# Performance work log

Measured on AMD Instinct MI355X. Metric: run time of the kernel, lower is better.

## Reference

```python
import jax, jax.numpy as jnp
import numpy as np

H = 64       # hidden size hard-coded in the module
NH = 4       # n_heads
S = 500      # stock_num
D = 10       # num_day
T = 40       # num_text (news per day)
FP = 3       # price features
FT = 512     # text embedding dim


def gru_scan(x, Wih, Whh, bih, bhh):
    """Single-sequence GRU (torch gate convention). x: (T, F) -> hidden states (T, H)."""
    gi = x @ Wih + bih  # (T, 3H) precompute input gates outside the scan

    def step(h, g):
        gh = h @ Whh + bhh
        r = jax.nn.sigmoid(g[:H] + gh[:H])
        z = jax.nn.sigmoid(g[H:2 * H] + gh[H:2 * H])
        n = jnp.tanh(g[2 * H:] + r * gh[2 * H:])
        h_new = (1.0 - z) * n + z * h
        return h_new, h_new

    h0 = jnp.zeros((H,), x.dtype)
    _, hs = jax.lax.scan(step, h0, gi)
    return hs


def attn_pool(hs, W, v):
    """Additive attention pooling over time. hs: (T, H) -> (H,)."""
    scores = jnp.tanh(hs @ W) @ v          # (T,)
    alpha = jax.nn.softmax(scores)
    return alpha @ hs


def _gru_params(key, fin, scale=0.08):
    k1, k2, k3, k4 = jax.random.split(key, 4)
    return (jax.random.normal(k1, (S, fin, 3 * H)) * scale,
            jax.random.normal(k2, (S, H, 3 * H)) * scale,
            jax.random.normal(k3, (S, 3 * H)) * scale,
            jax.random.normal(k4, (S, 3 * H)) * scale)


def _attn_params(key, scale=0.08):
    k1, k2 = jax.random.split(key)
    return (jax.random.normal(k1, (S, H, H)) * scale,
            jax.random.normal(k2, (S, H)) * scale)


def setup_inputs() -> dict:
    key = jax.random.key(0)
    ks = jax.random.split(key, 20)
    inp = {}
    inp['text_input'] = jax.random.normal(ks[0], (S, D, T, FT), dtype=jnp.float32)
    inp['price_input'] = jax.random.normal(ks[1], (S, D, FP), dtype=jnp.float32)
    inp['label'] = jax.random.randint(ks[2], (S,), 0, 2)
    inp['adj'] = jnp.ones((S, S), dtype=jnp.float32)
    inp['train'] = 0
    # per-stock stacked parameters
    (inp['Wih_p'], inp['Whh_p'], inp['bih_p'], inp['bhh_p']) = _gru_params(ks[3], FP)
    (inp['Wa_p'], inp['va_p']) = _attn_params(ks[4])
    (inp['Wih_t'], inp['Whh_t'], inp['bih_t'], inp['bhh_t']) = _gru_params(ks[5], FT)
    (inp['Wa_t'], inp['va_t']) = _attn_params(ks[6])
    (inp['Wih_s'], inp['Whh_s'], inp['bih_s'], inp['bhh_s']) = _gru_params(ks[7], H)
    (inp['Wa_s'], inp['va_s']) = _attn_params(ks[8])
    inp['Wb'] = jax.random.normal(ks[9], (S, H, H, H)) * 0.05   # Bilinear weight (out,in1,in2)
    inp['bb'] = jax.random.normal(ks[10], (S, H)) * 0.05
    inp['Wbl'] = jax.random.normal(ks[11], (S, H, 2)) * 0.08
    inp['bbl'] = jax.random.normal(ks[12], (S, 2)) * 0.08
    # shared cross-stock self-attention projections and final fc
    inp['Wq'] = jax.random.normal(ks[13], (H, H)) * 0.08
    inp['bq'] = jax.random.normal(ks[14], (H,)) * 0.08
    inp['Wk'] = jax.random.normal(ks[15], (H, H)) * 0.08
    inp['bk'] = jax.random.normal(ks[16], (H,)) * 0.08
    inp['Wf'] = jax.random.normal(ks[17], (H, 2)) * 0.08
    inp['bf'] = jax.random.normal(ks[18], (2,)) * 0.08
    return inp


def _forward(text_input, price_input, label,
             Wih_p, Whh_p, bih_p, bhh_p, Wa_p, va_p,
             Wih_t, Whh_t, bih_t, bhh_t, Wa_t, va_t,
             Wih_s, Whh_s, bih_s, bhh_s, Wa_s, va_s,
             Wb, bb, Wbl, bbl, Wq, bq, Wk, bk, Wf, bf):
    # ---- per-stock price encoder: GRU over days + attention pooling ----
    def enc_price(x, a, b, c, d, W, v):
        return attn_pool(gru_scan(x, a, b, c, d), W, v)
    x_price = jax.vmap(enc_price)(price_input, Wih_p, Whh_p, bih_p, bhh_p, Wa_p, va_p)  # (S, H)

    # ---- per-stock, per-day text encoder ----
    def enc_text_stock(xdays, a, b, c, d, W, v):
        return jax.vmap(lambda x: attn_pool(gru_scan(x, a, b, c, d), W, v))(xdays)  # (D, H)
    news = jax.vmap(enc_text_stock)(text_input, Wih_t, Whh_t, bih_t, bhh_t, Wa_t, va_t)  # (S, D, H)

    # ---- per-stock sequence encoder over days ----
    text_vec = jax.vmap(enc_price)(news, Wih_s, Whh_s, bih_s, bhh_s, Wa_s, va_s)  # (S, H)

    # ---- bilinear fusion: tanh(Bilinear(text, price)) ----
    combined = jnp.tanh(jnp.einsum('si,skij,sj->sk', text_vec, Wb, x_price) + bb)  # (S, H)

    # ---- per-stock blending head ----
    out_1 = jnp.tanh(jnp.einsum('si,sik->sk', combined, Wbl) + bbl)  # (S, 2)

    # ---- cross-stock multi-head self-attention (q,k projected, v identity) ----
    dh = H // NH
    q = (combined @ Wq + bq).reshape(S, NH, dh)
    k = (combined @ Wk + bk).reshape(S, NH, dh)
    v = combined.reshape(S, NH, dh)
    scores = jnp.einsum('shd,thd->hst', q, k) / (dh ** 0.5)
    attn = jax.nn.softmax(scores, axis=-1)
    attn_out = jnp.einsum('hst,thd->shd', attn, v).reshape(S, H)

    x = jax.nn.elu(attn_out @ Wf + bf)  # (S, 2)
    output = jax.nn.softmax(x + out_1, axis=1)
    # faithful to the original: CrossEntropyLoss applied to already-softmaxed output
    logp = jax.nn.log_softmax(output, axis=1)
    loss = -jnp.mean(logp[jnp.arange(S), label])
    return loss, output


def reference(text_input, price_input, label, adj, train,
              Wih_p, Whh_p, bih_p, bhh_p, Wa_p, va_p,
              Wih_t, Whh_t, bih_t, bhh_t, Wa_t, va_t,
              Wih_s, Whh_s, bih_s, bhh_s, Wa_s, va_s,
              Wb, bb, Wbl, bbl, Wq, bq, Wk, bk, Wf, bf):
    return _forward(text_input, price_input, label,
                    Wih_p, Whh_p, bih_p, bhh_p, Wa_p, va_p,
                    Wih_t, Whh_t, bih_t, bhh_t, Wa_t, va_t,
                    Wih_s, Whh_s, bih_s, bhh_s, Wa_s, va_s,
                    Wb, bb, Wbl, bbl, Wq, bq, Wk, bk, Wf, bf)
```

## Files before the change

kernel.cpp:

```cpp
#include <hip/hip_runtime.h>

#define Sn 500
#define Dn 10
#define Tn 40
#define FPn 3
#define FTn 512
#define Hn 64
#define G3 192
#define NHn 4

typedef __attribute__((ext_vector_type(8))) short bf8_t;
typedef __attribute__((ext_vector_type(4))) float f4_t;

__device__ __forceinline__ unsigned short f2bf(float f) {
    union { float f; unsigned int u; } v; v.f = f;
    unsigned int r = v.u + 0x7fffu + ((v.u >> 16) & 1u);
    return (unsigned short)(r >> 16);
}
__device__ __forceinline__ float bflo(unsigned int u) {
    union { unsigned int u; float f; } v; v.u = u << 16; return v.f;
}
__device__ __forceinline__ float bfhi(unsigned int u) {
    union { unsigned int u; float f; } v; v.u = u & 0xffff0000u; return v.f;
}
__device__ __forceinline__ unsigned int cvtpk(float lo, float hi) {
    unsigned int r;
    asm("v_cvt_pk_bf16_f32 %0, %1, %2" : "=v"(r) : "v"(lo), "v"(hi));
    return r;
}
__device__ __forceinline__ float sigmoidf_(float x) { return 1.f / (1.f + __expf(-x)); }
__device__ __forceinline__ float tanhf_(float x) {
    x = fminf(15.f, fmaxf(-15.f, x));
    float e = __expf(2.f * x);
    return (e - 1.f) / (e + 1.f);
}
__device__ __forceinline__ float dot8(uint4 wv, f4_t hA, f4_t hB) {
    return bflo(wv.x) * hA[0] + bfhi(wv.x) * hA[1]
         + bflo(wv.y) * hA[2] + bfhi(wv.y) * hA[3]
         + bflo(wv.z) * hB[0] + bfhi(wv.z) * hB[1]
         + bflo(wv.w) * hB[2] + bfhi(wv.w) * hB[3];
}
union bfu { bf8_t v; unsigned int u[4]; };

__global__ __launch_bounds__(256) void wih_prep(
    const float* __restrict__ Wih, unsigned short* __restrict__ wt)
{
    __shared__ float tile[64][65];
    const int bid = blockIdx.x;
    const int s = bid / 24, tlo = bid % 24;
    const int kt = tlo / 3, ct = tlo % 3;
    const int k0 = kt * 64, c0 = ct * 64;
    const int tid = threadIdx.x;

    const int c = tid & 63, r0 = tid >> 6;
    const float* src = Wih + ((size_t)s * FTn + k0) * G3 + c0 + c;
    #pragma unroll
    for (int i = 0; i < 16; ++i) {
        int r = i * 4 + r0;
        tile[c][r] = src[(size_t)r * G3];
    }
    __syncthreads();

    const int cl = tid >> 5, k2 = (tid & 31) * 2;
    unsigned int* wout = (unsigned int*)(wt + ((size_t)s * G3 + c0) * FTn + k0);
    #pragma unroll
    for (int p = 0; p < 8; ++p) {
        int col = cl + p * 8;
        wout[col * 256 + (k2 >> 1)] = cvtpk(tile[col][k2], tile[col][k2 + 1]);
    }
}

__global__ __launch_bounds__(256) void gi_gemm6(
    const float* __restrict__ text, const unsigned short* __restrict__ wt,
    const float* __restrict__ bih, float* __restrict__ gi2)
{
    __shared__ __align__(16) float Ab[2][2560];

    const int bid = blockIdx.x;
    const int xcd = bid & 7, ix = bid >> 3;
    const int swz = (xcd < 4 ? xcd * 313 : 1252 + (xcd - 4) * 312) + ix;
    const int s = swz / 5, fi = swz % 5;
    const int tid = threadIdx.x, w = tid >> 6, l = tid & 63;
    const int lr = l & 15, kg = l >> 4;

    const float* xbase = text + ((size_t)s * 400 + fi * 80) * FTn;
    const unsigned short* wtb = wt + ((size_t)s * G3 + w * 48) * FTn;

    const int c0 = tid, c1 = tid + 256, c2 = tid + 512;

    auto aload = [&](int kk, int c) -> f4_t {
        int row = c >> 3, slot = c & 7;
        return *(const f4_t*)(xbase + (size_t)row * FTn + kk * 32 + slot * 4);
    };
    auto awrite = [&](int c, f4_t v, float* buf) {
        int row = c >> 3, slot = c & 7;
        *(f4_t*)(buf + row * 32 + ((slot ^ (row & 7)) * 4)) = v;
    };
    auto afrag = [&](const float* buf, int mt) -> bf8_t {
        int row = mt * 16 + lr;
        int sw = row & 7;
        f4_t x0 = *(const f4_t*)(buf + row * 32 + ((((kg << 1)) ^ sw) << 2));
        f4_t x1 = *(const f4_t*)(buf + row * 32 + ((((kg << 1) | 1) ^ sw) << 2));
        bfu t;
        t.u[0] = cvtpk(x0[0], x0[1]); t.u[1] = cvtpk(x0[2], x0[3]);
        t.u[2] = cvtpk(x1[0], x1[1]); t.u[3] = cvtpk(x1[2], x1[3]);
        return t.v;
    };
    auto bload = [&](int kk, int nc) -> bf8_t {
        return *(const bf8_t*)(wtb + (size_t)(nc * 16 + lr) * FTn + kk * 32 + kg * 8);
    };

    f4_t acc[5][3];
    #pragma unroll
    for (int a = 0; a < 5; a++)
        #pragma unroll
        for (int b = 0; b < 3; b++) acc[a][b] = (f4_t){0.f, 0.f, 0.f, 0.f};

    f4_t a0 = aload(0, c0), a1 = aload(0, c1), a2;
    if (tid < 128) a2 = aload(0, c2);
    bf8_t bc0 = bload(0, 0), bc1 = bload(0, 1), bc2 = bload(0, 2);
    awrite(c0, a0, Ab[0]); awrite(c1, a1, Ab[0]);
    if (tid < 128) awrite(c2, a2, Ab[0]);
    __syncthreads();

    bf8_t bn0 = bc0, bn1 = bc1, bn2 = bc2;
    for (int kk = 0; kk < 16; ++kk) {
        float* cur = Ab[kk & 1];
        float* nxt = Ab[(kk & 1) ^ 1];
        if (kk < 15) {
            a0 = aload(kk + 1, c0); a1 = aload(kk + 1, c1);
            if (tid < 128) a2 = aload(kk + 1, c2);
            bn0 = bload(kk + 1, 0); bn1 = bload(kk + 1, 1); bn2 = bload(kk + 1, 2);
        }
        #pragma unroll
        for (int mt = 0; mt < 5; ++mt) {
            bf8_t af = afrag(cur, mt);
            acc[mt][0] = __builtin_amdgcn_mfma_f32_16x16x32_bf16(af, bc0, acc[mt][0], 0, 0, 0);
            acc[mt][1] = __builtin_amdgcn_mfma_f32_16x16x32_bf16(af, bc1, acc[mt][1], 0, 0, 0);
            acc[mt][2] = __builtin_amdgcn_mfma_f32_16x16x32_bf16(af, bc2, acc[mt][2], 0, 0, 0);
        }
        if (kk < 15) {
            awrite(c0, a0, nxt); awrite(c1, a1, nxt);
            if (tid < 128) awrite(c2, a2, nxt);
        }
        __syncthreads();
        bc0 = bn0; bc1 = bn1; bc2 = bn2;
    }

    const float* bihs = bih + (size_t)s * G3 + w * 48 + lr;
    #pragma unroll
    for (int nc = 0; nc < 3; ++nc) {
        const int col = w * 48 + nc * 16 + lr;
        const float bv = bihs[nc * 16];
        #pragma unroll
        for (int mt = 0; mt < 5; ++mt)
            #pragma unroll
            for (int rg = 0; rg < 4; ++rg) {
                int r = mt * 16 + kg * 4 + rg;
                int hi = (r >= 40);
                int day = fi * 2 + hi;
                int t = r - hi * 40;
                gi2[((size_t)(s * 40 + t) * 10 + day) * 192 + col] = acc[mt][nc][rg] + bv;
            }
    }
}

__global__ __launch_bounds__(64, 1) void gru_text_f(
    const float* __restrict__ gi2, const float* __restrict__ Whh,
    const float* __restrict__ bhh, const float* __restrict__ Wa,
    const float* __restrict__ va, float* __restrict__ news)
{
    __shared__ __align__(16) float hrow[16 * 68];
    __shared__ __align__(16) unsigned char waT[Hn * 128];

    const int s = blockIdx.x, l = threadIdx.x;
    const int lr = l & 15, lg = l >> 4;

    const float* Whhs = Whh + (size_t)s * Hn * G3;
    bfu bwhh[2][12];
    #pragma unroll
    for (int ks = 0; ks < 2; ++ks)
        #pragma unroll
        for (int nt = 0; nt < 12; ++nt) {
            const float* p = Whhs + (size_t)(ks * 32 + lg * 8) * G3 + nt * 16 + lr;
            float b0 = p[0], b1 = p[G3], b2 = p[2 * G3], b3 = p[3 * G3];
            float b4 = p[4 * G3], b5 = p[5 * G3], b6 = p[6 * G3], b7 = p[7 * G3];
            bwhh[ks][nt].u[0] = cvtpk(b0, b1); bwhh[ks][nt].u[1] = cvtpk(b2, b3);
            bwhh[ks][nt].u[2] = cvtpk(b4, b5); bwhh[ks][nt].u[3] = cvtpk(b6, b7);
        }
    float bhh_l[12];
    #pragma unroll
    for (int nt = 0; nt < 12; ++nt) bhh_l[nt] = bhh[(size_t)s * G3 + nt * 16 + lr];
    float va_l[4];
    #pragma unroll
    for (int nt = 0; nt < 4; ++nt) va_l[nt] = va[(size_t)s * Hn + nt * 16 + lr];

    {
        const float* Was = Wa + (size_t)s * Hn * Hn;
        for (int r = 0; r < 64; ++r) {
            int e = l + r * 64, i = e >> 6, k = e & 63;
            *(unsigned short*)(waT + k * 128 + ((2 * i) ^ ((k & 7) << 4))) = f2bf(Was[e]);
        }
        #pragma unroll
        for (int r = 0; r < 17; ++r) hrow[l + r * 64] = 0.f;
    }
    __builtin_amdgcn_wave_barrier();

    int dayoff[4];
    #pragma unroll
    for (int rr = 0; rr < 4; ++rr) {
        int d = lg * 4 + rr; if (d > 9) d = 9;
        dayoff[rr] = d * 192 + lr;
    }
    const float* gbase = gi2 + (size_t)s * 40 * 1920;

    float val[48], valn[48];
    #pragma unroll
    for (int j = 0; j < 48; ++j) val[j] = gbase[dayoff[j & 3] + (j >> 2) * 16];

    bf8_t a0f, a1f;
    {   bfu z0; z0.u[0] = 0; z0.u[1] = 0; z0.u[2] = 0; z0.u[3] = 0; a0f = z0.v; a1f = z0.v; }

    float h[4][4], accv[4][4], den[4], m[4];
    #pragma unroll
    for (int nt = 0; nt < 4; ++nt)
        #pragma unroll
        for (int rr = 0; rr < 4; ++rr) { h[nt][rr] = 0.f; accv[nt][rr] = 0.f; }
    #pragma unroll
    for (int rr = 0; rr < 4; ++rr) { den[rr] = 0.f; m[rr] = -1e30f; }

    for (int t = 0; t < Tn; ++t) {
        f4_t acc[12];
        #pragma unroll
        for (int nt = 0; nt < 12; ++nt)
            acc[nt] = (f4_t){bhh_l[nt], bhh_l[nt], bhh_l[nt], bhh_l[nt]};
        #pragma unroll
        for (int nt = 0; nt < 12; ++nt) {
            acc[nt] = __builtin_amdgcn_mfma_f32_16x16x32_bf16(a0f, bwhh[0][nt].v, acc[nt], 0, 0, 0);
            acc[nt] = __builtin_amdgcn_mfma_f32_16x16x32_bf16(a1f, bwhh[1][nt].v, acc[nt], 0, 0, 0);
        }
        {
            const int tn = (t < Tn - 1) ? t + 1 : t;
            const float* gb = gbase + (size_t)tn * 1920;
            #pragma unroll
            for (int j = 0; j < 48; ++j) valn[j] = gb[dayoff[j & 3] + (j >> 2) * 16];
        }
        #pragma unroll
        for (int nt = 0; nt < 4; ++nt)
            #pragma unroll
            for (int rr = 0; rr < 4; ++rr) {
                float r = sigmoidf_(val[nt * 4 + rr] + acc[nt][rr]);
                float z = sigmoidf_(val[(nt + 4) * 4 + rr] + acc[nt + 4][rr]);
                float n = tanhf_(val[(nt + 8) * 4 + rr] + r * acc[nt + 8][rr]);
                h[nt][rr] = (1.f - z) * n + z * h[nt][rr];
            }
        __builtin_amdgcn_wave_barrier();
        #pragma unroll
        for (int rr = 0; rr < 4; ++rr) {
            int day = lg * 4 + rr;
            if (day < Dn) {
                #pragma unroll
                for (int nt = 0; nt < 4; ++nt) hrow[day * 68 + nt * 16 + lr] = h[nt][rr];
            }
        }
        __builtin_amdgcn_wave_barrier();
        {
            const float* hp = hrow + lr * 68 + lg * 8;
            f4_t x0 = *(const f4_t*)hp,        x1 = *(const f4_t*)(hp + 4);
            f4_t y0 = *(const f4_t*)(hp + 32), y1 = *(const f4_t*)(hp + 36);
            bfu t0, t1;
            t0.u[0] = cvtpk(x0[0], x0[1]); t0.u[1] = cvtpk(x0[2], x0[3]);
            t0.u[2] = cvtpk(x1[0], x1[1]); t0.u[3] = cvtpk(x1[2], x1[3]);
            t1.u[0] = cvtpk(y0[0], y0[1]); t1.u[1] = cvtpk(y0[2], y0[3]);
            t1.u[2] = cvtpk(y1[0], y1[1]); t1.u[3] = cvtpk(y1[2], y1[3]);
            a0f = t0.v; a1f = t1.v;
        }
        f4_t sc[4];
        #pragma unroll
        for (int nt = 0; nt < 4; ++nt) sc[nt] = (f4_t){0.f, 0.f, 0.f, 0.f};
        #pragma unroll
        for (int ks = 0; ks < 2; ++ks) {
            bf8_t av = ks ? a1f : a0f;
            #pragma unroll
            for (int nt = 0; nt < 4; ++nt) {
                bf8_t bwv = *(const bf8_t*)(waT + (nt * 16 + lr) * 128
                                            + ((ks * 64 + lg * 16) ^ ((lr & 7) << 4)));
                sc[nt] = __builtin_amdgcn_mfma_f32_16x16x32_bf16(av, bwv, sc[nt], 0, 0, 0);
            }
        }
        float pr[4];
        #pragma unroll
        for (int rr = 0; rr < 4; ++rr) {
            pr[rr] = tanhf_(sc[0][rr]) * va_l[0] + tanhf_(sc[1][rr]) * va_l[1]
                   + tanhf_(sc[2][rr]) * va_l[2] + tanhf_(sc[3][rr]) * va_l[3];
            pr[rr] += __shfl_xor(pr[rr], 1);
            pr[rr] += __shfl_xor(pr[rr], 2);
            pr[rr] += __shfl_xor(pr[rr], 4);
            pr[rr] += __shfl_xor(pr[rr], 8);
        }
        #pragma unroll
        for (int rr = 0; rr < 4; ++rr) {
            float mn = fmaxf(m[rr], pr[rr]);
            float s0 = __expf(m[rr] - mn);
            float p = __expf(pr[rr] - mn);
            den[rr] = den[rr] * s0 + p;
            #pragma unroll
            for (int nt = 0; nt < 4; ++nt)
                accv[nt][rr] = accv[nt][rr] * s0 + p * h[nt][rr];
            m[rr] = mn;
        }
        #pragma unroll
        for (int j = 0; j < 48; ++j) val[j] = valn[j];
    }
    #pragma unroll
    for (int rr = 0; rr < 4; ++rr) {
        int day = lg * 4 + rr;
        if (day < Dn) {
            float inv = 1.f / den[rr];
            #pragma unroll
            for (int nt = 0; nt < 4; ++nt)
                news[((size_t)s * Dn + day) * Hn + nt * 16 + lr] = accv[nt][rr] * inv;
        }
    }
}

__global__ __launch_bounds__(64, 1) void gru_small_f(
    const float* __restrict__ news,
    const float* __restrict__ Wih_s, const float* __restrict__ Whh_s,
    const float* __restrict__ bih_s, const float* __restrict__ bhh_s,
    const float* __restrict__ Wa_s, const float* __restrict__ va_s,
    const float* __restrict__ price, const float* __restrict__ Wih_p,
    const float* __restrict__ Whh_p, const float* __restrict__ bih_p,
    const float* __restrict__ bhh_p, const float* __restrict__ Wa_p,
    const float* __restrict__ va_p,
    float* __restrict__ tvec, float* __restrict__ xprice)
{
    __shared__ __align__(16) unsigned char sm[60928];
    unsigned char* whh2 = sm;
    unsigned char* wih2 = sm + 24576;
    unsigned char* wa2 = sm + 49152;
    float* newsL = (float*)(sm + 57600);
    float* hbuf  = (float*)(sm + 60320);
    float* priceL = (float*)(sm + 60608);

    const int s = blockIdx.x, l = threadIdx.x;

    {
        const float* W2 = Whh_s + (size_t)s * Hn * G3;
        const float* X2 = Wih_s + (size_t)s * Hn * G3;
        for (int r = 0; r < 192; ++r) {
            int e = l + r * 64, i = e / G3, j = e - i * G3;
            int off = j * 128 + ((2 * i) ^ ((j & 7) << 4));
            *(unsigned short*)(whh2 + off) = f2bf(W2[e]);
            *(unsigned short*)(wih2 + off) = f2bf(X2[e]);
        }
        const float* A2 = Wa_s + (size_t)s * Hn * Hn;
        for (int r = 0; r < 64; ++r) {
            int e = l + r * 64, i = e >> 6, k = e & 63;
            *(unsigned short*)(wa2 + k * 128 + ((2 * i) ^ ((k & 7) << 4))) = f2bf(A2[e]);
        }
        #pragma unroll
        for (int d = 0; d < Dn; ++d) newsL[d * 68 + l] = news[((size_t)s * Dn + d) * Hn + l];
        hbuf[l] = 0.f;
        if (l < 4) hbuf[64 + l] = 0.f;
    }
    __builtin_amdgcn_wave_barrier();
    {
        const float bi0 = bih_s[(size_t)s * G3 + l];
        const float bi1 = bih_s[(size_t)s * G3 + 64 + l];
        const float bi2 = bih_s[(size_t)s * G3 + 128 + l];
        const float bh0 = bhh_s[(size_t)s * G3 + l];
        const float bh1 = bhh_s[(size_t)s * G3 + 64 + l];
        const float bh2 = bhh_s[(size_t)s * G3 + 128 + l];
        const float vak = va_s[(size_t)s * Hn + l];
        const int swl = (l & 7) << 4;
        float h2 = 0.f, m2 = -1e30f, den2 = 0.f, av2 = 0.f;
        for (int t = 0; t < Dn; ++t) {
            float gh0 = bh0, gh1 = bh1, gh2 = bh2;
            float gg0 = bi0, gg1 = bi1, gg2 = bi2;
            #pragma unroll
            for (int ic = 0; ic < 8; ++ic) {
                const int off = (ic * 16) ^ swl;
                f4_t hA = *(const f4_t*)&hbuf[ic * 8];
                f4_t hB = *(const f4_t*)&hbuf[ic * 8 + 4];
                f4_t nA = *(const f4_t*)&newsL[t * 68 + ic * 8];
                f4_t nB = *(const f4_t*)&newsL[t * 68 + ic * 8 + 4];
                uint4 w0 = *(const uint4*)(whh2 + l * 128 + off);
                uint4 w1 = *(const uint4*)(whh2 + (l + 64) * 128 + off);
                uint4 w2 = *(const uint4*)(whh2 + (l + 128) * 128 + off);
                uint4 x0 = *(const uint4*)(wih2 + l * 128 + off);
                uint4 x1 = *(const uint4*)(wih2 + (l + 64) * 128 + off);
                uint4 x2 = *(const uint4*)(wih2 + (l + 128) * 128 + off);
                gh0 += dot8(w0, hA, hB); gh1 += dot8(w1, hA, hB); gh2 += dot8(w2, hA, hB);
                gg0 += dot8(x0, nA, nB); gg1 += dot8(x1, nA, nB); gg2 += dot8(x2, nA, nB);
            }
            float r = sigmoidf_(gg0 + gh0);
            float z = sigmoidf_(gg1 + gh1);
            float n = tanhf_(gg2 + r * gh2);
            h2 = (1.f - z) * n + z * h2;
            __builtin_amdgcn_wave_barrier();
            hbuf[l] = h2;
            __builtin_amdgcn_wave_barrier();
            float sk = 0.f;
            #pragma unroll
            for (int ic = 0; ic < 8; ++ic) {
                const int off = (ic * 16) ^ swl;
                uint4 wv = *(const uint4*)(wa2 + l * 128 + off);
                f4_t hA = *(const f4_t*)&hbuf[ic * 8];
                f4_t hB = *(const f4_t*)&hbuf[ic * 8 + 4];
                sk += dot8(wv, hA, hB);
            }
            float term = tanhf_(sk) * vak;
            #pragma unroll
            for (int off = 32; off; off >>= 1) term += __shfl_xor(term, off);
            float mn = fmaxf(m2, term);
            float s0 = __expf(m2 - mn);
            float p = __expf(term - mn);
            den2 = den2 * s0 + p;
            av2 = av2 * s0 + p * h2;
            m2 = mn;
        }
        tvec[(size_t)s * Hn + l] = av2 / den2;
    }
    __builtin_amdgcn_wave_barrier();

    {
        const float* W3 = Whh_p + (size_t)s * Hn * G3;
        for (int r = 0; r < 192; ++r) {
            int e = l + r * 64, i = e / G3, j = e - i * G3;
            *(unsigned short*)(whh2 + j * 128 + ((2 * i) ^ ((j & 7) << 4))) = f2bf(W3[e]);
        }
        const float* A3 = Wa_p + (size_t)s * Hn * Hn;
        for (int r = 0; r < 64; ++r) {
            int e = l + r * 64, i = e >> 6, k = e & 63;
            *(unsigned short*)(wa2 + k * 128 + ((2 * i) ^ ((k & 7) << 4))) = f2bf(A3[e]);
        }
        if (l < 30) priceL[l] = price[(size_t)s * 30 + l];
        hbuf[l] = 0.f;
        if (l < 4) hbuf[64 + l] = 0.f;
    }
    __builtin_amdgcn_wave_barrier();
    {
        float wp[3][3];
        #pragma unroll
        for (int i = 0; i < 3; ++i)
            #pragma unroll
            for (int g = 0; g < 3; ++g)
                wp[i][g] = Wih_p[(size_t)s * 3 * G3 + i * G3 + g * 64 + l];
        const float bi0 = bih_p[(size_t)s * G3 + l];
        const float bi1 = bih_p[(size_t)s * G3 + 64 + l];
        const float bi2 = bih_p[(size_t)s * G3 + 128 + l];
        const float bh0 = bhh_p[(size_t)s * G3 + l];
        const float bh1 = bhh_p[(size_t)s * G3 + 64 + l];
        const float bh2 = bhh_p[(size_t)s * G3 + 128 + l];
        const float vak = va_p[(size_t)s * Hn + l];
        const int swl = (l & 7) << 4;
        float h3 = 0.f, m3 = -1e30f, den3 = 0.f, av3 = 0.f;
        for (int t = 0; t < Dn; ++t) {
            float x0 = priceL[t * 3], x1 = priceL[t * 3 + 1], x2 = priceL[t * 3 + 2];
            float gg0 = bi0 + x0 * wp[0][0] + x1 * wp[1][0] + x2 * wp[2][0];
            float gg1 = bi1 + x0 * wp[0][1] + x1 * wp[1][1] + x2 * wp[2][1];
            float gg2 = bi2 + x0 * wp[0][2] + x1 * wp[1][2] + x2 * wp[2][2];
            float gh0 = bh0, gh1 = bh1, gh2 = bh2;
            #pragma unroll
            for (int ic = 0; ic < 8; ++ic) {
                const int off = (ic * 16) ^ swl;
                f4_t hA = *(const f4_t*)&hbuf[ic * 8];
                f4_t hB = *(const f4_t*)&hbuf[ic * 8 + 4];
                uint4 w0 = *(const uint4*)(whh2 + l * 128 + off);
                uint4 w1 = *(const uint4*)(whh2 + (l + 64) * 128 + off);
                uint4 w2 = *(const uint4*)(whh2 + (l + 128) * 128 + off);
                gh0 += dot8(w0, hA, hB); gh1 += dot8(w1, hA, hB); gh2 += dot8(w2, hA, hB);
            }
            float r = sigmoidf_(gg0 + gh0);
            float z = sigmoidf_(gg1 + gh1);
            float n = tanhf_(gg2 + r * gh2);
            h3 = (1.f - z) * n + z * h3;
            __builtin_amdgcn_wave_barrier();
            hbuf[l] = h3;
            __builtin_amdgcn_wave_barrier();
            float sk = 0.f;
            #pragma unroll
            for (int ic = 0; ic < 8; ++ic) {
                const int off = (ic * 16) ^ swl;
                uint4 wv = *(const uint4*)(wa2 + l * 128 + off);
                f4_t hA = *(const f4_t*)&hbuf[ic * 8];
                f4_t hB = *(const f4_t*)&hbuf[ic * 8 + 4];
                sk += dot8(wv, hA, hB);
            }
            float term = tanhf_(sk) * vak;
            #pragma unroll
            for (int off = 32; off; off >>= 1) term += __shfl_xor(term, off);
            float mn = fmaxf(m3, term);
            float s0 = __expf(m3 - mn);
            float p = __expf(term - mn);
            den3 = den3 * s0 + p;
            av3 = av3 * s0 + p * h3;
            m3 = mn;
        }
        xprice[(size_t)s * Hn + l] = av3 / den3;
    }
}

__global__ __launch_bounds__(256) void bilinear4(
    const float* __restrict__ Wb, const float* __restrict__ bb,
    const float* __restrict__ xprice, const float* __restrict__ tvec,
    float* __restrict__ combined)
{
    __shared__ __align__(16) float uT[Hn][16];
    __shared__ float tv[Hn];

    const int bid = blockIdx.x, s = bid >> 2, kq = bid & 3;
    const int tid = threadIdx.x;
    const int w = tid >> 6, l = tid & 63;
    if (tid < Hn) tv[tid] = tvec[s * Hn + tid];
    const int j4 = (l & 15) * 4;
    f4_t xq = *(const f4_t*)&xprice[s * Hn + j4];
    __syncthreads();

    const float* Wbs = Wb + (size_t)s * Hn * Hn * Hn;
    for (int g = 0; g < 64; ++g) {
        int P = kq * 1024 + w * 256 + g * 4 + (l >> 4);
        f4_t wv = *(const f4_t*)&Wbs[(size_t)P * Hn + j4];
        float dp = wv[0] * xq[0] + wv[1] * xq[1] + wv[2] * xq[2] + wv[3] * xq[3];
        dp += __shfl_xor(dp, 8);
        dp += __shfl_xor(dp, 4);
        dp += __shfl_xor(dp, 2);
        dp += __shfl_xor(dp, 1);
        if ((l & 15) == 0) { int k = P >> 6, i = P & 63; uT[i][k - kq * 16] = dp; }
    }
    __syncthreads();
    if (tid < 16) {
        const int k = kq * 16 + tid;
        float a = bb[s * Hn + k];
        for (int i = 0; i < Hn; i++) a += tv[i] * uT[i][tid];
        combined[s * Hn + k] = tanhf_(a);
    }
}

__global__ __launch_bounds__(64) void qk_proj(
    const float* __restrict__ combined, const float* __restrict__ Wq,
    const float* __restrict__ bq, const float* __restrict__ Wk,
    const float* __restrict__ bk, const float* __restrict__ Wbl,
    const float* __restrict__ bbl,
    float* __restrict__ qg, float* __restrict__ kg, float* __restrict__ out1)
{
    __shared__ float cl[Hn];
    const int s = blockIdx.x, l = threadIdx.x;
    cl[l] = combined[s * Hn + l];
    __syncthreads();
    float aq = bq[l], ak = bk[l];
    for (int i = 0; i < Hn; i++) {
        float ci = cl[i];
        aq += ci * Wq[i * Hn + l];
        ak += ci * Wk[i * Hn + l];
    }
    qg[s * Hn + l] = aq; kg[s * Hn + l] = ak;
    if (l < 2) {
        float a = bbl[s * 2 + l];
        for (int i = 0; i < Hn; i++) a += cl[i] * Wbl[(size_t)s * Hn * 2 + i * 2 + l];
        out1[s * 2 + l] = tanhf_(a);
    }
}

__global__ __launch_bounds__(256) void mhsa(
    const float* __restrict__ qg, const float* __restrict__ kg,
    const float* __restrict__ combined, const float* __restrict__ Wf,
    const float* __restrict__ bfp, const float* __restrict__ out1,
    float* __restrict__ dout)
{
    __shared__ __align__(16) float ql[Hn];
    __shared__ float sl[NHn][Sn];
    __shared__ float hsum[NHn];
    __shared__ float ao[Hn];
    __shared__ float red2[8];
    __shared__ float red3[4][Hn];

    const int sq = blockIdx.x, tid = threadIdx.x;
    if (tid < Hn) ql[tid] = qg[sq * Hn + tid];
    __syncthreads();

    for (int id = tid; id < Sn * NHn; id += 256) {
        int t = id >> 2, h = id & 3;
        const float* kp = &kg[t * Hn + h * 16];
        float a = 0.f;
        #pragma unroll
        for (int x = 0; x < 16; x += 4) {
            f4_t kv = *(const f4_t*)&kp[x];
            f4_t qv = *(const f4_t*)&ql[h * 16 + x];
            a += kv[0] * qv[0] + kv[1] * qv[1] + kv[2] * qv[2] + kv[3] * qv[3];
        }
        sl[h][t] = a * 0.25f;
    }
    __syncthreads();
    for (int h = 0; h < NHn; ++h) {
        float m = -1e30f;
        for (int t = tid; t < Sn; t += 256) m = fmaxf(m, sl[h][t]);
        for (int o = 32; o; o >>= 1) m = fmaxf(m, __shfl_xor(m, o));
        if ((tid & 63) == 0) red2[tid >> 6] = m;
        __syncthreads();
        m = fmaxf(fmaxf(red2[0], red2[1]), fmaxf(red2[2], red2[3]));
        float ps = 0.f;
        for (int t = tid; t < Sn; t += 256) { float p = __expf(sl[h][t] - m); sl[h][t] = p; ps += p; }
        for (int o = 32; o; o >>= 1) ps += __shfl_xor(ps, o);
        if ((tid & 63) == 0) red2[4 + (tid >> 6)] = ps;
        __syncthreads();
        if (tid == 0) hsum[h] = red2[4] + red2[5] + red2[6] + red2[7];
        __syncthreads();
    }
    {
        const int q = tid >> 6, j = tid & 63, h = j >> 4;
        float a = 0.f;
        for (int t = q * 125; t < q * 125 + 125; ++t) a += sl[h][t] * combined[t * Hn + j];
        red3[q][j] = a;
    }
    __syncthreads();
    if (tid < Hn)
        ao[tid] = (red3[0][tid] + red3[1][tid] + red3[2][tid] + red3[3][tid]) / hsum[tid >> 4];
    __syncthreads();
    if (tid == 0) {
        float l0 = bfp[0], l1 = bfp[1];
        for (int j = 0; j < Hn; j++) { float v = ao[j]; l0 += v * Wf[j * 2]; l1 += v * Wf[j * 2 + 1]; }
        l0 = l0 > 0.f ? l0 : __expf(l0) - 1.f;
        l1 = l1 > 0.f ? l1 : __expf(l1) - 1.f;
        l0 += out1[sq * 2]; l1 += out1[sq * 2 + 1];
        float m = fmaxf(l0, l1);
        float e0 = __expf(l0 - m), e1 = __expf(l1 - m);
        float inv = 1.f / (e0 + e1);
        dout[1 + sq * 2] = e0 * inv;
        dout[2 + sq * 2] = e1 * inv;
    }
}

__global__ __launch_bounds__(512) void loss_k(float* __restrict__ dout,
                                              const int* __restrict__ label)
{
    __shared__ float red[512];
    const int tid = threadIdx.x;
    float a = 0.f;
    if (tid < Sn) {
        float p0 = dout[1 + 2 * tid], p1 = dout[2 + 2 * tid];
        float m = fmaxf(p0, p1);
        float lse = m + __logf(__expf(p0 - m) + __expf(p1 - m));
        float pl = label[tid] ? p1 : p0;
        a = -(pl - lse);
    }
    red[tid] = a;
    __syncthreads();
    for (int o = 256; o; o >>= 1) {
        if (tid < o) red[tid] += red[tid + o];
        __syncthreads();
    }
    if (tid == 0) dout[0] = red[0] / (float)Sn;
}

extern "C" void kernel_launch(void* const* d_in, const int* in_sizes, int n_in,
                              void* d_out, int out_size, void* d_ws, size_t ws_size,
                              hipStream_t stream)
{
    const float* text  = (const float*)d_in[0];
    const float* price = (const float*)d_in[1];
    const int*   label = (const int*)  d_in[2];
    const float* Wih_p = (const float*)d_in[5];
    const float* Whh_p = (const float*)d_in[6];
    const float* bih_p = (const float*)d_in[7];
    const float* bhh_p = (const float*)d_in[8];
    const float* Wa_p  = (const float*)d_in[9];
    const float* va_p  = (const float*)d_in[10];
    const float* Wih_t = (const float*)d_in[11];
    const float* Whh_t = (const float*)d_in[12];
    const float* bih_t = (const float*)d_in[13];
    const float* bhh_t = (const float*)d_in[14];
    const float* Wa_t  = (const float*)d_in[15];
    const float* va_t  = (const float*)d_in[16];
    const float* Wih_s = (const float*)d_in[17];
    const float* Whh_s = (const float*)d_in[18];
    const float* bih_s = (const float*)d_in[19];
    const float* bhh_s = (const float*)d_in[20];
    const float* Wa_s  = (const float*)d_in[21];
    const float* va_s  = (const float*)d_in[22];
    const float* Wb    = (const float*)d_in[23];
    const float* bb    = (const float*)d_in[24];
    const float* Wbl   = (const float*)d_in[25];
    const float* bbl   = (const float*)d_in[26];
    const float* Wq    = (const float*)d_in[27];
    const float* bq    = (const float*)d_in[28];
    const float* Wk    = (const float*)d_in[29];
    const float* bk    = (const float*)d_in[30];
    const float* Wf    = (const float*)d_in[31];
    const float* bf_   = (const float*)d_in[32];

    float* ws = (float*)d_ws;
    float* news     = ws;
    float* xprice   = ws + 320000;
    float* tvec     = ws + 352000;
    float* combined = ws + 384000;
    float* qg       = ws + 416000;
    float* kg       = ws + 448000;
    float* out1     = ws + 480000;
    float* gi2      = ws + 481000;
    unsigned short* wt = (unsigned short*)(ws + 481000 + 38400000);
    float* dout = (float*)d_out;

    wih_prep<<<Sn * 24, 256, 0, stream>>>(Wih_t, wt);
    gi_gemm6<<<Sn * 5, 256, 0, stream>>>(text, wt, bih_t, gi2);
    gru_text_f<<<Sn, 64, 0, stream>>>(gi2, Whh_t, bhh_t, Wa_t, va_t, news);
    gru_small_f<<<Sn, 64, 0, stream>>>(news,
                                       Wih_s, Whh_s, bih_s, bhh_s, Wa_s, va_s,
                                       price, Wih_p, Whh_p, bih_p, bhh_p, Wa_p, va_p,
                                       tvec, xprice);
    bilinear4<<<Sn * 4, 256, 0, stream>>>(Wb, bb, xprice, tvec, combined);
    qk_proj<<<Sn, 64, 0, stream>>>(combined, Wq, bq, Wk, bk, Wbl, bbl, qg, kg, out1);
    mhsa<<<Sn, 256, 0, stream>>>(qg, kg, combined, Wf, bf_, out1, dout);
    loss_k<<<1, 512, 0, stream>>>(dout, label);
}
```

Baseline: 644.6 us.

## Fuse prep, GEMM, bilinear and projection kernels; precompute bilinear u off the recurrence path

```diff
diff --git a/kernel.cpp b/kernel.cpp
--- a/kernel.cpp
+++ b/kernel.cpp
@@ -42,387 +42,51 @@
 }
 union bfu { bf8_t v; unsigned int u[4]; };
 
-__global__ __launch_bounds__(256) void wih_prep(
-    const float* __restrict__ Wih, unsigned short* __restrict__ wt)
-{
-    __shared__ float tile[64][65];
-    const int bid = blockIdx.x;
-    const int s = bid / 24, tlo = bid % 24;
-    const int kt = tlo / 3, ct = tlo % 3;
-    const int k0 = kt * 64, c0 = ct * 64;
-    const int tid = threadIdx.x;
-
-    const int c = tid & 63, r0 = tid >> 6;
-    const float* src = Wih + ((size_t)s * FTn + k0) * G3 + c0 + c;
-    #pragma unroll
-    for (int i = 0; i < 16; ++i) {
-        int r = i * 4 + r0;
-        tile[c][r] = src[(size_t)r * G3];
-    }
-    __syncthreads();
-
-    const int cl = tid >> 5, k2 = (tid & 31) * 2;
-    unsigned int* wout = (unsigned int*)(wt + ((size_t)s * G3 + c0) * FTn + k0);
-    #pragma unroll
-    for (int p = 0; p < 8; ++p) {
-        int col = cl + p * 8;
-        wout[col * 256 + (k2 >> 1)] = cvtpk(tile[col][k2], tile[col][k2 + 1]);
-    }
-}
-
-__global__ __launch_bounds__(256) void gi_gemm6(
-    const float* __restrict__ text, const unsigned short* __restrict__ wt,
-    const float* __restrict__ bih, float* __restrict__ gi2)
-{
-    __shared__ __align__(16) float Ab[2][2560];
-
-    const int bid = blockIdx.x;
-    const int xcd = bid & 7, ix = bid >> 3;
-    const int swz = (xcd < 4 ? xcd * 313 : 1252 + (xcd - 4) * 312) + ix;
-    const int s = swz / 5, fi = swz % 5;
-    const int tid = threadIdx.x, w = tid >> 6, l = tid & 63;
-    const int lr = l & 15, kg = l >> 4;
-
-    const float* xbase = text + ((size_t)s * 400 + fi * 80) * FTn;
-    const unsigned short* wtb = wt + ((size_t)s * G3 + w * 48) * FTn;
-
-    const int c0 = tid, c1 = tid + 256, c2 = tid + 512;
-
-    auto aload = [&](int kk, int c) -> f4_t {
-        int row = c >> 3, slot = c & 7;
-        return *(const f4_t*)(xbase + (size_t)row * FTn + kk * 32 + slot * 4);
-    };
-    auto awrite = [&](int c, f4_t v, float* buf) {
-        int row = c >> 3, slot = c & 7;
-        *(f4_t*)(buf + row * 32 + ((slot ^ (row & 7)) * 4)) = v;
-    };
-    auto afrag = [&](const float* buf, int mt) -> bf8_t {
-        int row = mt * 16 + lr;
-        int sw = row & 7;
-        f4_t x0 = *(const f4_t*)(buf + row * 32 + ((((kg << 1)) ^ sw) << 2));
-        f4_t x1 = *(const f4_t*)(buf + row * 32 + ((((kg << 1) | 1) ^ sw) << 2));
-        bfu t;
-        t.u[0] = cvtpk(x0[0], x0[1]); t.u[1] = cvtpk(x0[2], x0[3]);
-        t.u[2] = cvtpk(x1[0], x1[1]); t.u[3] = cvtpk(x1[2], x1[3]);
-        return t.v;
-    };
-    auto bload = [&](int kk, int nc) -> bf8_t {
-        return *(const bf8_t*)(wtb + (size_t)(nc * 16 + lr) * FTn + kk * 32 + kg * 8);
-    };
-
-    f4_t acc[5][3];
-    #pragma unroll
-    for (int a = 0; a < 5; a++)
-        #pragma unroll
-        for (int b = 0; b < 3; b++) acc[a][b] = (f4_t){0.f, 0.f, 0.f, 0.f};
-
-    f4_t a0 = aload(0, c0), a1 = aload(0, c1), a2;
-    if (tid < 128) a2 = aload(0, c2);
-    bf8_t bc0 = bload(0, 0), bc1 = bload(0, 1), bc2 = bload(0, 2);
-    awrite(c0, a0, Ab[0]); awrite(c1, a1, Ab[0]);
-    if (tid < 128) awrite(c2, a2, Ab[0]);
-    __syncthreads();
-
-    bf8_t bn0 = bc0, bn1 = bc1, bn2 = bc2;
-    for (int kk = 0; kk < 16; ++kk) {
-        float* cur = Ab[kk & 1];
-        float* nxt = Ab[(kk & 1) ^ 1];
-        if (kk < 15) {
-            a0 = aload(kk + 1, c0); a1 = aload(kk + 1, c1);
-            if (tid < 128) a2 = aload(kk + 1, c2);
-            bn0 = bload(kk + 1, 0); bn1 = bload(kk + 1, 1); bn2 = bload(kk + 1, 2);
-        }
-        #pragma unroll
-        for (int mt = 0; mt < 5; ++mt) {
-            bf8_t af = afrag(cur, mt);
-            acc[mt][0] = __builtin_amdgcn_mfma_f32_16x16x32_bf16(af, bc0, acc[mt][0], 0, 0, 0);
-            acc[mt][1] = __builtin_amdgcn_mfma_f32_16x16x32_bf16(af, bc1, acc[mt][1], 0, 0, 0);
-            acc[mt][2] = __builtin_amdgcn_mfma_f32_16x16x32_bf16(af, bc2, acc[mt][2], 0, 0, 0);
-        }
-        if (kk < 15) {
-            awrite(c0, a0, nxt); awrite(c1, a1, nxt);
-            if (tid < 128) awrite(c2, a2, nxt);
-        }
-        __syncthreads();
-        bc0 = bn0; bc1 = bn1; bc2 = bn2;
-    }
-
-    const float* bihs = bih + (size_t)s * G3 + w * 48 + lr;
-    #pragma unroll
-    for (int nc = 0; nc < 3; ++nc) {
-        const int col = w * 48 + nc * 16 + lr;
-        const float bv = bihs[nc * 16];
-        #pragma unroll
-        for (int mt = 0; mt < 5; ++mt)
-            #pragma unroll
-            for (int rg = 0; rg < 4; ++rg) {
-                int r = mt * 16 + kg * 4 + rg;
-                int hi = (r >= 40);
-                int day = fi * 2 + hi;
-                int t = r - hi * 40;
-                gi2[((size_t)(s * 40 + t) * 10 + day) * 192 + col] = acc[mt][nc][rg] + bv;
-            }
-    }
-}
-
-__global__ __launch_bounds__(64, 1) void gru_text_f(
-    const float* __restrict__ gi2, const float* __restrict__ Whh,
-    const float* __restrict__ bhh, const float* __restrict__ Wa,
-    const float* __restrict__ va, float* __restrict__ news)
-{
-    __shared__ __align__(16) float hrow[16 * 68];
-    __shared__ __align__(16) unsigned char waT[Hn * 128];
-
-    const int s = blockIdx.x, l = threadIdx.x;
-    const int lr = l & 15, lg = l >> 4;
-
-    const float* Whhs = Whh + (size_t)s * Hn * G3;
-    bfu bwhh[2][12];
-    #pragma unroll
-    for (int ks = 0; ks < 2; ++ks)
-        #pragma unroll
-        for (int nt = 0; nt < 12; ++nt) {
-            const float* p = Whhs + (size_t)(ks * 32 + lg * 8) * G3 + nt * 16 + lr;
-            float b0 = p[0], b1 = p[G3], b2 = p[2 * G3], b3 = p[3 * G3];
-            float b4 = p[4 * G3], b5 = p[5 * G3], b6 = p[6 * G3], b7 = p[7 * G3];
-            bwhh[ks][nt].u[0] = cvtpk(b0, b1); bwhh[ks][nt].u[1] = cvtpk(b2, b3);
-            bwhh[ks][nt].u[2] = cvtpk(b4, b5); bwhh[ks][nt].u[3] = cvtpk(b6, b7);
-        }
-    float bhh_l[12];
-    #pragma unroll
-    for (int nt = 0; nt < 12; ++nt) bhh_l[nt] = bhh[(size_t)s * G3 + nt * 16 + lr];
-    float va_l[4];
-    #pragma unroll
-    for (int nt = 0; nt < 4; ++nt) va_l[nt] = va[(size_t)s * Hn + nt * 16 + lr];
-
-    {
-        const float* Was = Wa + (size_t)s * Hn * Hn;
-        for (int r = 0; r < 64; ++r) {
-            int e = l + r * 64, i = e >> 6, k = e & 63;
-            *(unsigned short*)(waT + k * 128 + ((2 * i) ^ ((k & 7) << 4))) = f2bf(Was[e]);
-        }
-        #pragma unroll
-        for (int r = 0; r < 17; ++r) hrow[l + r * 64] = 0.f;
-    }
-    __builtin_amdgcn_wave_barrier();
-
-    int dayoff[4];
-    #pragma unroll
-    for (int rr = 0; rr < 4; ++rr) {
-        int d = lg * 4 + rr; if (d > 9) d = 9;
-        dayoff[rr] = d * 192 + lr;
-    }
-    const float* gbase = gi2 + (size_t)s * 40 * 1920;
-
-    float val[48], valn[48];
-    #pragma unroll
-    for (int j = 0; j < 48; ++j) val[j] = gbase[dayoff[j & 3] + (j >> 2) * 16];
-
-    bf8_t a0f, a1f;
-    {   bfu z0; z0.u[0] = 0; z0.u[1] = 0; z0.u[2] = 0; z0.u[3] = 0; a0f = z0.v; a1f = z0.v; }
-
-    float h[4][4], accv[4][4], den[4], m[4];
-    #pragma unroll
-    for (int nt = 0; nt < 4; ++nt)
-        #pragma unroll
-        for (int rr = 0; rr < 4; ++rr) { h[nt][rr] = 0.f; accv[nt][rr] = 0.f; }
-    #pragma unroll
-    for (int rr = 0; rr < 4; ++rr) { den[rr] = 0.f; m[rr] = -1e30f; }
-
-    for (int t = 0; t < Tn; ++t) {
-        f4_t acc[12];
-        #pragma unroll
-        for (int nt = 0; nt < 12; ++nt)
-            acc[nt] = (f4_t){bhh_l[nt], bhh_l[nt], bhh_l[nt], bhh_l[nt]};
-        #pragma unroll
-        for (int nt = 0; nt < 12; ++nt) {
-            acc[nt] = __builtin_amdgcn_mfma_f32_16x16x32_bf16(a0f, bwhh[0][nt].v, acc[nt], 0, 0, 0);
-            acc[nt] = __builtin_amdgcn_mfma_f32_16x16x32_bf16(a1f, bwhh[1][nt].v, acc[nt], 0, 0, 0);
-        }
-        {
-            const int tn = (t < Tn - 1) ? t + 1 : t;
-            const float* gb = gbase + (size_t)tn * 1920;
-            #pragma unroll
-            for (int j = 0; j < 48; ++j) valn[j] = gb[dayoff[j & 3] + (j >> 2) * 16];
-        }
-        #pragma unroll
-        for (int nt = 0; nt < 4; ++nt)
-            #pragma unroll
-            for (int rr = 0; rr < 4; ++rr) {
-                float r = sigmoidf_(val[nt * 4 + rr] + acc[nt][rr]);
-                float z = sigmoidf_(val[(nt + 4) * 4 + rr] + acc[nt + 4][rr]);
-                float n = tanhf_(val[(nt + 8) * 4 + rr] + r * acc[nt + 8][rr]);
-                h[nt][rr] = (1.f - z) * n + z * h[nt][rr];
-            }
-        __builtin_amdgcn_wave_barrier();
-        #pragma unroll
-        for (int rr = 0; rr < 4; ++rr) {
-            int day = lg * 4 + rr;
-            if (day < Dn) {
-                #pragma unroll
-                for (int nt = 0; nt < 4; ++nt) hrow[day * 68 + nt * 16 + lr] = h[nt][rr];
-            }
-        }
-        __builtin_amdgcn_wave_barrier();
-        {
-            const float* hp = hrow + lr * 68 + lg * 8;
-            f4_t x0 = *(const f4_t*)hp,        x1 = *(const f4_t*)(hp + 4);
-            f4_t y0 = *(const f4_t*)(hp + 32), y1 = *(const f4_t*)(hp + 36);
-            bfu t0, t1;
-            t0.u[0] = cvtpk(x0[0], x0[1]); t0.u[1] = cvtpk(x0[2], x0[3]);
-            t0.u[2] = cvtpk(x1[0], x1[1]); t0.u[3] = cvtpk(x1[2], x1[3]);
-            t1.u[0] = cvtpk(y0[0], y0[1]); t1.u[1] = cvtpk(y0[2], y0[3]);
-            t1.u[2] = cvtpk(y1[0], y1[1]); t1.u[3] = cvtpk(y1[2], y1[3]);
-            a0f = t0.v; a1f = t1.v;
-        }
-        f4_t sc[4];
-        #pragma unroll
-        for (int nt = 0; nt < 4; ++nt) sc[nt] = (f4_t){0.f, 0.f, 0.f, 0.f};
-        #pragma unroll
-        for (int ks = 0; ks < 2; ++ks) {
-            bf8_t av = ks ? a1f : a0f;
-            #pragma unroll
-            for (int nt = 0; nt < 4; ++nt) {
-                bf8_t bwv = *(const bf8_t*)(waT + (nt * 16 + lr) * 128
-                                            + ((ks * 64 + lg * 16) ^ ((lr & 7) << 4)));
-                sc[nt] = __builtin_amdgcn_mfma_f32_16x16x32_bf16(av, bwv, sc[nt], 0, 0, 0);
-            }
-        }
-        float pr[4];
-        #pragma unroll
-        for (int rr = 0; rr < 4; ++rr) {
-            pr[rr] = tanhf_(sc[0][rr]) * va_l[0] + tanhf_(sc[1][rr]) * va_l[1]
-                   + tanhf_(sc[2][rr]) * va_l[2] + tanhf_(sc[3][rr]) * va_l[3];
-            pr[rr] += __shfl_xor(pr[rr], 1);
-            pr[rr] += __shfl_xor(pr[rr], 2);
-            pr[rr] += __shfl_xor(pr[rr], 4);
-            pr[rr] += __shfl_xor(pr[rr], 8);
-        }
-        #pragma unroll
-        for (int rr = 0; rr < 4; ++rr) {
-            float mn = fmaxf(m[rr], pr[rr]);
-            float s0 = __expf(m[rr] - mn);
-            float p = __expf(pr[rr] - mn);
-            den[rr] = den[rr] * s0 + p;
-            #pragma unroll
-            for (int nt = 0; nt < 4; ++nt)
-                accv[nt][rr] = accv[nt][rr] * s0 + p * h[nt][rr];
-            m[rr] = mn;
-        }
-        #pragma unroll
-        for (int j = 0; j < 48; ++j) val[j] = valn[j];
-    }
-    #pragma unroll
-    for (int rr = 0; rr < 4; ++rr) {
-        int day = lg * 4 + rr;
-        if (day < Dn) {
-            float inv = 1.f / den[rr];
-            #pragma unroll
-            for (int nt = 0; nt < 4; ++nt)
-                news[((size_t)s * Dn + day) * Hn + nt * 16 + lr] = accv[nt][rr] * inv;
-        }
-    }
-}
-
-__global__ __launch_bounds__(64, 1) void gru_small_f(
-    const float* __restrict__ news,
-    const float* __restrict__ Wih_s, const float* __restrict__ Whh_s,
-    const float* __restrict__ bih_s, const float* __restrict__ bhh_s,
-    const float* __restrict__ Wa_s, const float* __restrict__ va_s,
+__global__ __launch_bounds__(256) void prep_fused(
+    const float* __restrict__ Wih, unsigned short* __restrict__ wt,
     const float* __restrict__ price, const float* __restrict__ Wih_p,
     const float* __restrict__ Whh_p, const float* __restrict__ bih_p,
     const float* __restrict__ bhh_p, const float* __restrict__ Wa_p,
-    const float* __restrict__ va_p,
-    float* __restrict__ tvec, float* __restrict__ xprice)
+    const float* __restrict__ va_p, float* __restrict__ xprice)
 {
-    __shared__ __align__(16) unsigned char sm[60928];
-    unsigned char* whh2 = sm;
-    unsigned char* wih2 = sm + 24576;
-    unsigned char* wa2 = sm + 49152;
-    float* newsL = (float*)(sm + 57600);
-    float* hbuf  = (float*)(sm + 60320);
-    float* priceL = (float*)(sm + 60608);
-
-    const int s = blockIdx.x, l = threadIdx.x;
-
-    {
-        const float* W2 = Whh_s + (size_t)s * Hn * G3;
-        const float* X2 = Wih_s + (size_t)s * Hn * G3;
-        for (int r = 0; r < 192; ++r) {
-            int e = l + r * 64, i = e / G3, j = e - i * G3;
-            int off = j * 128 + ((2 * i) ^ ((j & 7) << 4));
-            *(unsigned short*)(whh2 + off) = f2bf(W2[e]);
-            *(unsigned short*)(wih2 + off) = f2bf(X2[e]);
-        }
-        const float* A2 = Wa_s + (size_t)s * Hn * Hn;
-        for (int r = 0; r < 64; ++r) {
-            int e = l + r * 64, i = e >> 6, k = e & 63;
-            *(unsigned short*)(wa2 + k * 128 + ((2 * i) ^ ((k & 7) << 4))) = f2bf(A2[e]);
-        }
-        #pragma unroll
-        for (int d = 0; d < Dn; ++d) newsL[d * 68 + l] = news[((size_t)s * Dn + d) * Hn + l];
-        hbuf[l] = 0.f;
-        if (l < 4) hbuf[64 + l] = 0.f;
-    }
-    __builtin_amdgcn_wave_barrier();
-    {
-        const float bi0 = bih_s[(size_t)s * G3 + l];
-        const float bi1 = bih_s[(size_t)s * G3 + 64 + l];
-        const float bi2 = bih_s[(size_t)s * G3 + 128 + l];
-        const float bh0 = bhh_s[(size_t)s * G3 + l];
-        const float bh1 = bhh_s[(size_t)s * G3 + 64 + l];
-        const float bh2 = bhh_s[(size_t)s * G3 + 128 + l];
-        const float vak = va_s[(size_t)s * Hn + l];
-        const int swl = (l & 7) << 4;
-        float h2 = 0.f, m2 = -1e30f, den2 = 0.f, av2 = 0.f;
-        for (int t = 0; t < Dn; ++t) {
-            float gh0 = bh0, gh1 = bh1, gh2 = bh2;
-            float gg0 = bi0, gg1 = bi1, gg2 = bi2;
-            #pragma unroll
-            for (int ic = 0; ic < 8; ++ic) {
-                const int off = (ic * 16) ^ swl;
-                f4_t hA = *(const f4_t*)&hbuf[ic * 8];
-                f4_t hB = *(const f4_t*)&hbuf[ic * 8 + 4];
-                f4_t nA = *(const f4_t*)&newsL[t * 68 + ic * 8];
-                f4_t nB = *(const f4_t*)&newsL[t * 68 + ic * 8 + 4];
-                uint4 w0 = *(const uint4*)(whh2 + l * 128 + off);
-                uint4 w1 = *(const uint4*)(whh2 + (l + 64) * 128 + off);
-                uint4 w2 = *(const uint4*)(whh2 + (l + 128) * 128 + off);
-                uint4 x0 = *(const uint4*)(wih2 + l * 128 + off);
-                uint4 x1 = *(const uint4*)(wih2 + (l + 64) * 128 + off);
-                uint4 x2 = *(const uint4*)(wih2 + (l + 128) * 128 + off);
-                gh0 += dot8(w0, hA, hB); gh1 += dot8(w1, hA, hB); gh2 += dot8(w2, hA, hB);
-                gg0 += dot8(x0, nA, nB); gg1 += dot8(x1, nA, nB); gg2 += dot8(x2, nA, nB);
-            }
-            float r = sigmoidf_(gg0 + gh0);
-            float z = sigmoidf_(gg1 + gh1);
-            float n = tanhf_(gg2 + r * gh2);
-            h2 = (1.f - z) * n + z * h2;
-            __builtin_amdgcn_wave_barrier();
-            hbuf[l] = h2;
-            __builtin_amdgcn_wave_barrier();
-            float sk = 0.f;
-            #pragma unroll
-            for (int ic = 0; ic < 8; ++ic) {
-                const int off = (ic * 16) ^ swl;
-                uint4 wv = *(const uint4*)(wa2 + l * 128 + off);
-                f4_t hA = *(const f4_t*)&hbuf[ic * 8];
-                f4_t hB = *(const f4_t*)&hbuf[ic * 8 + 4];
-                sk += dot8(wv, hA, hB);
-            }
-            float term = tanhf_(sk) * vak;
-            #pragma unroll
-            for (int off = 32; off; off >>= 1) term += __shfl_xor(term, off);
-            float mn = fmaxf(m2, term);
-            float s0 = __expf(m2 - mn);
-            float p = __expf(term - mn);
-            den2 = den2 * s0 + p;
-            av2 = av2 * s0 + p * h2;
-            m2 = mn;
-        }
-        tvec[(size_t)s * Hn + l] = av2 / den2;
-    }
-    __builtin_amdgcn_wave_barrier();
+    __shared__ float tile[64][65];
+    __shared__ __align__(16) unsigned char smp[33160];
+
+    const int bid = blockIdx.x, tid = threadIdx.x;
+
+    if (bid < 12000) {
+        const int s = bid / 24, tlo = bid % 24;
+        const int kt = tlo / 3, ct = tlo % 3;
+        const int k0 = kt * 64, c0 = ct * 64;
+
+        const int c = tid & 63, r0 = tid >> 6;
+        const float* src = Wih + ((size_t)s * FTn + k0) * G3 + c0 + c;
+        #pragma unroll
+        for (int i = 0; i < 16; ++i) {
+            int r = i * 4 + r0;
+            tile[c][r] = src[(size_t)r * G3];
+        }
+        __syncthreads();
+
+        const int cl = tid >> 5, k2 = (tid & 31) * 2;
+        unsigned int* wo = (unsigned int*)wt;
+        const int kc = (k0 >> 3) + (k2 >> 3), e2 = (k2 & 7) >> 1;
+        #pragma unroll
+        for (int p = 0; p < 8; ++p) {
+            int col = cl + p * 8;
+            wo[(size_t)s * 49152 + ((size_t)kc * G3 + c0 + col) * 4 + e2] =
+                cvtpk(tile[col][k2], tile[col][k2 + 1]);
+        }
+        return;
+    }
+
+    const int s = bid - 12000;
+    if (tid >= 64) return;
+    const int l = tid;
+    unsigned char* whh2 = smp;
+    unsigned char* wa2 = smp + 24576;
+    float* hbuf = (float*)(smp + 32768);
+    float* priceL = (float*)(smp + 33040);
 
     {
         const float* W3 = Whh_p + (size_t)s * Hn * G3;
@@ -502,64 +166,441 @@
     }
 }
 
-__global__ __launch_bounds__(256) void bilinear4(
-    const float* __restrict__ Wb, const float* __restrict__ bb,
-    const float* __restrict__ xprice, const float* __restrict__ tvec,
-    float* __restrict__ combined)
+__global__ __launch_bounds__(256) void main_fused(
+    const float* __restrict__ text, const unsigned short* __restrict__ wt,
+    const float* __restrict__ bih, float* __restrict__ gi2,
+    const float* __restrict__ Wb, const float* __restrict__ xprice,
+    float* __restrict__ u)
 {
-    __shared__ __align__(16) float uT[Hn][16];
-    __shared__ float tv[Hn];
-
-    const int bid = blockIdx.x, s = bid >> 2, kq = bid & 3;
-    const int tid = threadIdx.x;
-    const int w = tid >> 6, l = tid & 63;
-    if (tid < Hn) tv[tid] = tvec[s * Hn + tid];
-    const int j4 = (l & 15) * 4;
-    f4_t xq = *(const f4_t*)&xprice[s * Hn + j4];
-    __syncthreads();
-
-    const float* Wbs = Wb + (size_t)s * Hn * Hn * Hn;
-    for (int g = 0; g < 64; ++g) {
-        int P = kq * 1024 + w * 256 + g * 4 + (l >> 4);
-        f4_t wv = *(const f4_t*)&Wbs[(size_t)P * Hn + j4];
-        float dp = wv[0] * xq[0] + wv[1] * xq[1] + wv[2] * xq[2] + wv[3] * xq[3];
-        dp += __shfl_xor(dp, 8);
-        dp += __shfl_xor(dp, 4);
-        dp += __shfl_xor(dp, 2);
-        dp += __shfl_xor(dp, 1);
-        if ((l & 15) == 0) { int k = P >> 6, i = P & 63; uT[i][k - kq * 16] = dp; }
-    }
-    __syncthreads();
-    if (tid < 16) {
-        const int k = kq * 16 + tid;
-        float a = bb[s * Hn + k];
-        for (int i = 0; i < Hn; i++) a += tv[i] * uT[i][tid];
-        combined[s * Hn + k] = tanhf_(a);
-    }
-}
-
-__global__ __launch_bounds__(64) void qk_proj(
-    const float* __restrict__ combined, const float* __restrict__ Wq,
-    const float* __restrict__ bq, const float* __restrict__ Wk,
-    const float* __restrict__ bk, const float* __restrict__ Wbl,
-    const float* __restrict__ bbl,
-    float* __restrict__ qg, float* __restrict__ kg, float* __restrict__ out1)
+    __shared__ __align__(16) unsigned char sm[20480];
+
+    const int id = blockIdx.x;
+    const int grp = id / 9, sub = id - grp * 9;
+    const int tid = threadIdx.x, w = tid >> 6, l = tid & 63;
+
+    if (sub < 5) {
+        const int s = grp, fi = sub;
+        const int lr = l & 15, kg = l >> 4;
+        unsigned short* Ab0 = (unsigned short*)sm;
+        unsigned short* Ab1 = Ab0 + 5120;
+
+        const float* xbase = text + ((size_t)s * 400 + fi * 80) * FTn;
+        const unsigned short* wtb = wt + (size_t)s * 98304 + (size_t)(w * 48 + lr) * 8;
+
+        const int c0 = tid, c1 = tid + 256, c2 = tid + 512;
+
+        f4_t acc[5][3];
+        #pragma unroll
+        for (int a = 0; a < 5; a++)
+            #pragma unroll
+            for (int b = 0; b < 3; b++) acc[a][b] = (f4_t){0.f, 0.f, 0.f, 0.f};
+
+        f4_t pa[3], pb[3];
+        auto aload = [&](int kk) {
+            #pragma unroll
+            for (int q = 0; q < 3; ++q) {
+                int c = tid + q * 256;
+                if (q < 2 || tid < 128) {
+                    int row = c >> 3, slot = c & 7;
+                    const float* p = xbase + (size_t)row * FTn + kk * 64 + slot * 8;
+                    pa[q] = *(const f4_t*)p; pb[q] = *(const f4_t*)(p + 4);
+                }
+            }
+        };
+        auto awrite = [&](unsigned short* buf) {
+            #pragma unroll
+            for (int q = 0; q < 3; ++q) {
+                int c = tid + q * 256;
+                if (q < 2 || tid < 128) {
+                    int row = c >> 3, slot = c & 7;
+                    uint4 uu = { cvtpk(pa[q][0], pa[q][1]), cvtpk(pa[q][2], pa[q][3]),
+                                 cvtpk(pb[q][0], pb[q][1]), cvtpk(pb[q][2], pb[q][3]) };
+                    *(uint4*)(buf + row * 64 + ((slot ^ (row & 7)) * 8)) = uu;
+                }
+            }
+        };
+        auto bload = [&](int kk, int ks, int nc) -> bf8_t {
+            return *(const bf8_t*)(wtb + (size_t)((kk * 8 + ks * 4 + kg) * G3 + nc * 16) * 8);
+        };
+        auto afrag = [&](const unsigned short* buf, int mt, int ks) -> bf8_t {
+            int row = mt * 16 + lr;
+            int slot = (ks * 4 + kg) ^ (row & 7);
+            return *(const bf8_t*)(buf + row * 64 + slot * 8);
+        };
+
+        bf8_t bc[2][3], bn[2][3];
+        aload(0);
+        #pragma unroll
+        for (int ks = 0; ks < 2; ++ks)
+            #pragma unroll
+            for (int nc = 0; nc < 3; ++nc) bc[ks][nc] = bload(0, ks, nc);
+        awrite(Ab0);
+        __syncthreads();
+
+        for (int kk = 0; kk < 8; ++kk) {
+            unsigned short* cur = (kk & 1) ? Ab1 : Ab0;
+            unsigned short* nxt = (kk & 1) ? Ab0 : Ab1;
+            if (kk < 7) {
+                aload(kk + 1);
+                #pragma unroll
+                for (int ks = 0; ks < 2; ++ks)
+                    #pragma unroll
+                    for (int nc = 0; nc < 3; ++nc) bn[ks][nc] = bload(kk + 1, ks, nc);
+            }
+            #pragma unroll
+            for (int ks = 0; ks < 2; ++ks)
+                #pragma unroll
+                for (int mt = 0; mt < 5; ++mt) {
+                    bf8_t af = afrag(cur, mt, ks);
+                    acc[mt][0] = __builtin_amdgcn_mfma_f32_16x16x32_bf16(af, bc[ks][0], acc[mt][0], 0, 0, 0);
+                    acc[mt][1] = __builtin_amdgcn_mfma_f32_16x16x32_bf16(af, bc[ks][1], acc[mt][1], 0, 0, 0);
+                    acc[mt][2] = __builtin_amdgcn_mfma_f32_16x16x32_bf16(af, bc[ks][2], acc[mt][2], 0, 0, 0);
+                }
+            if (kk < 7) awrite(nxt);
+            __syncthreads();
+            #pragma unroll
+            for (int ks = 0; ks < 2; ++ks)
+                #pragma unroll
+                for (int nc = 0; nc < 3; ++nc) bc[ks][nc] = bn[ks][nc];
+        }
+
+        const float* bihs = bih + (size_t)s * G3 + w * 48 + lr;
+        #pragma unroll
+        for (int nc = 0; nc < 3; ++nc) {
+            const int col = w * 48 + nc * 16 + lr;
+            const float bv = bihs[nc * 16];
+            #pragma unroll
+            for (int mt = 0; mt < 5; ++mt)
+                #pragma unroll
+                for (int rg = 0; rg < 4; ++rg) {
+                    int r = mt * 16 + kg * 4 + rg;
+                    int hi = (r >= 40);
+                    int day = fi * 2 + hi;
+                    int t = r - hi * 40;
+                    gi2[((size_t)(s * 40 + t) * 10 + day) * 192 + col] = acc[mt][nc][rg] + bv;
+                }
+        }
+    } else {
+        const int s = grp, kq = sub - 5;
+        float* uT = (float*)sm;
+        const int j4 = (l & 15) * 4;
+        f4_t xq = *(const f4_t*)&xprice[s * Hn + j4];
+
+        const float* Wbs = Wb + (size_t)s * Hn * Hn * Hn;
+        for (int g = 0; g < 64; ++g) {
+            int P = kq * 1024 + w * 256 + g * 4 + (l >> 4);
+            f4_t wv = *(const f4_t*)&Wbs[(size_t)P * Hn + j4];
+            float dp = wv[0] * xq[0] + wv[1] * xq[1] + wv[2] * xq[2] + wv[3] * xq[3];
+            dp += __shfl_xor(dp, 8);
+            dp += __shfl_xor(dp, 4);
+            dp += __shfl_xor(dp, 2);
+            dp += __shfl_xor(dp, 1);
+            if ((l & 15) == 0) { int k = P >> 6, i = P & 63; uT[i * 17 + (k - kq * 16)] = dp; }
+        }
+        __syncthreads();
+        #pragma unroll
+        for (int r = 0; r < 4; ++r) {
+            int flat = tid + r * 256;
+            int kr = flat >> 6, i = flat & 63;
+            u[((size_t)s * 64 + kq * 16 + kr) * 64 + i] = uT[i * 17 + kr];
+        }
+    }
+}
+
+__global__ __launch_bounds__(64, 1) void gru_text_f(
+    const float* __restrict__ gi2, const float* __restrict__ Whh,
+    const float* __restrict__ bhh, const float* __restrict__ Wa,
+    const float* __restrict__ va, float* __restrict__ news)
 {
-    __shared__ float cl[Hn];
+    __shared__ __align__(16) float hrow[16 * 68];
+    __shared__ __align__(16) unsigned char waT[Hn * 128];
+
     const int s = blockIdx.x, l = threadIdx.x;
-    cl[l] = combined[s * Hn + l];
-    __syncthreads();
-    float aq = bq[l], ak = bk[l];
-    for (int i = 0; i < Hn; i++) {
-        float ci = cl[i];
-        aq += ci * Wq[i * Hn + l];
-        ak += ci * Wk[i * Hn + l];
-    }
-    qg[s * Hn + l] = aq; kg[s * Hn + l] = ak;
-    if (l < 2) {
-        float a = bbl[s * 2 + l];
-        for (int i = 0; i < Hn; i++) a += cl[i] * Wbl[(size_t)s * Hn * 2 + i * 2 + l];
-        out1[s * 2 + l] = tanhf_(a);
+    const int lr = l & 15, lg = l >> 4;
+
+    const float* Whhs = Whh + (size_t)s * Hn * G3;
+    bfu bwhh[2][12];
+    #pragma unroll
+    for (int ks = 0; ks < 2; ++ks)
+        #pragma unroll
+        for (int nt = 0; nt < 12; ++nt) {
+            const float* p = Whhs + (size_t)(ks * 32 + lg * 8) * G3 + nt * 16 + lr;
+            float b0 = p[0], b1 = p[G3], b2 = p[2 * G3], b3 = p[3 * G3];
+            float b4 = p[4 * G3], b5 = p[5 * G3], b6 = p[6 * G3], b7 = p[7 * G3];
+            bwhh[ks][nt].u[0] = cvtpk(b0, b1); bwhh[ks][nt].u[1] = cvtpk(b2, b3);
+            bwhh[ks][nt].u[2] = cvtpk(b4, b5); bwhh[ks][nt].u[3] = cvtpk(b6, b7);
+        }
+    float bhh_l[12];
+    #pragma unroll
+    for (int nt = 0; nt < 12; ++nt) bhh_l[nt] = bhh[(size_t)s * G3 + nt * 16 + lr];
+    float va_l[4];
+    #pragma unroll
+    for (int nt = 0; nt < 4; ++nt) va_l[nt] = va[(size_t)s * Hn + nt * 16 + lr];
+
+    {
+        const float* Was = Wa + (size_t)s * Hn * Hn;
+        for (int r = 0; r < 64; ++r) {
+            int e = l + r * 64, i = e >> 6, k = e & 63;
+            *(unsigned short*)(waT + k * 128 + ((2 * i) ^ ((k & 7) << 4))) = f2bf(Was[e]);
+        }
+        #pragma unroll
+        for (int r = 0; r < 17; ++r) hrow[l + r * 64] = 0.f;
+    }
+    __builtin_amdgcn_wave_barrier();
+
+    int dayoff[4];
+    #pragma unroll
+    for (int rr = 0; rr < 4; ++rr) {
+        int d = lg * 4 + rr; if (d > 9) d = 9;
+        dayoff[rr] = d * 192 + lr;
+    }
+    const float* gbase = gi2 + (size_t)s * 40 * 1920;
+
+    float val[48], valn[48];
+    #pragma unroll
+    for (int j = 0; j < 48; ++j) val[j] = gbase[dayoff[j & 3] + (j >> 2) * 16];
+
+    bf8_t a0f, a1f;
+    {   bfu z0; z0.u[0] = 0; z0.u[1] = 0; z0.u[2] = 0; z0.u[3] = 0; a0f = z0.v; a1f = z0.v; }
+
+    float h[4][4], accv[4][4], den[4], m[4];
+    #pragma unroll
+    for (int nt = 0; nt < 4; ++nt)
+        #pragma unroll
+        for (int rr = 0; rr < 4; ++rr) { h[nt][rr] = 0.f; accv[nt][rr] = 0.f; }
+    #pragma unroll
+    for (int rr = 0; rr < 4; ++rr) { den[rr] = 0.f; m[rr] = -1e30f; }
+
+    for (int t = 0; t < Tn; ++t) {
+        f4_t acc[12];
+        #pragma unroll
+        for (int nt = 0; nt < 12; ++nt)
+            acc[nt] = (f4_t){bhh_l[nt], bhh_l[nt], bhh_l[nt], bhh_l[nt]};
+        __builtin_amdgcn_s_setprio(1);
+        #pragma unroll
+        for (int nt = 0; nt < 12; ++nt) {
+            acc[nt] = __builtin_amdgcn_mfma_f32_16x16x32_bf16(a0f, bwhh[0][nt].v, acc[nt], 0, 0, 0);
+            acc[nt] = __builtin_amdgcn_mfma_f32_16x16x32_bf16(a1f, bwhh[1][nt].v, acc[nt], 0, 0, 0);
+        }
+        __builtin_amdgcn_s_setprio(0);
+        {
+            const int tn = (t < Tn - 1) ? t + 1 : t;
+            const float* gb = gbase + (size_t)tn * 1920;
+            #pragma unroll
+            for (int j = 0; j < 48; ++j) valn[j] = gb[dayoff[j & 3] + (j >> 2) * 16];
+        }
+        #pragma unroll
+        for (int nt = 0; nt < 4; ++nt)
+            #pragma unroll
+            for (int rr = 0; rr < 4; ++rr) {
+                float r = sigmoidf_(val[nt * 4 + rr] + acc[nt][rr]);
+                float z = sigmoidf_(val[(nt + 4) * 4 + rr] + acc[nt + 4][rr]);
+                float n = tanhf_(val[(nt + 8) * 4 + rr] + r * acc[nt + 8][rr]);
+                h[nt][rr] = (1.f - z) * n + z * h[nt][rr];
+            }
+        __builtin_amdgcn_wave_barrier();
+        #pragma unroll
+        for (int rr = 0; rr < 4; ++rr) {
+            int day = lg * 4 + rr;
+            if (day < Dn) {
+                #pragma unroll
+                for (int nt = 0; nt < 4; ++nt) hrow[day * 68 + nt * 16 + lr] = h[nt][rr];
+            }
+        }
+        __builtin_amdgcn_wave_barrier();
+        {
+            const float* hp = hrow + lr * 68 + lg * 8;
+            f4_t x0 = *(const f4_t*)hp,        x1 = *(const f4_t*)(hp + 4);
+            f4_t y0 = *(const f4_t*)(hp + 32), y1 = *(const f4_t*)(hp + 36);
+            bfu t0, t1;
+            t0.u[0] = cvtpk(x0[0], x0[1]); t0.u[1] = cvtpk(x0[2], x0[3]);
+            t0.u[2] = cvtpk(x1[0], x1[1]); t0.u[3] = cvtpk(x1[2], x1[3]);
+            t1.u[0] = cvtpk(y0[0], y0[1]); t1.u[1] = cvtpk(y0[2], y0[3]);
+            t1.u[2] = cvtpk(y1[0], y1[1]); t1.u[3] = cvtpk(y1[2], y1[3]);
+            a0f = t0.v; a1f = t1.v;
+        }
+        f4_t sc[4];
+        #pragma unroll
+        for (int nt = 0; nt < 4; ++nt) sc[nt] = (f4_t){0.f, 0.f, 0.f, 0.f};
+        __builtin_amdgcn_s_setprio(1);
+        #pragma unroll
+        for (int ks = 0; ks < 2; ++ks) {
+            bf8_t av = ks ? a1f : a0f;
+            #pragma unroll
+            for (int nt = 0; nt < 4; ++nt) {
+                bf8_t bwv = *(const bf8_t*)(waT + (nt * 16 + lr) * 128
+                                            + ((ks * 64 + lg * 16) ^ ((lr & 7) << 4)));
+                sc[nt] = __builtin_amdgcn_mfma_f32_16x16x32_bf16(av, bwv, sc[nt], 0, 0, 0);
+            }
+        }
+        __builtin_amdgcn_s_setprio(0);
+        float pr[4];
+        #pragma unroll
+        for (int rr = 0; rr < 4; ++rr) {
+            pr[rr] = tanhf_(sc[0][rr]) * va_l[0] + tanhf_(sc[1][rr]) * va_l[1]
+                   + tanhf_(sc[2][rr]) * va_l[2] + tanhf_(sc[3][rr]) * va_l[3];
+            pr[rr] += __shfl_xor(pr[rr], 1);
+            pr[rr] += __shfl_xor(pr[rr], 2);
+            pr[rr] += __shfl_xor(pr[rr], 4);
+            pr[rr] += __shfl_xor(pr[rr], 8);
+        }
+        #pragma unroll
+        for (int rr = 0; rr < 4; ++rr) {
+            float mn = fmaxf(m[rr], pr[rr]);
+            float s0 = __expf(m[rr] - mn);
+            float p = __expf(pr[rr] - mn);
+            den[rr] = den[rr] * s0 + p;
+            #pragma unroll
+            for (int nt = 0; nt < 4; ++nt)
+                accv[nt][rr] = accv[nt][rr] * s0 + p * h[nt][rr];
+            m[rr] = mn;
+        }
+        #pragma unroll
+        for (int j = 0; j < 48; ++j) val[j] = valn[j];
+    }
+    #pragma unroll
+    for (int rr = 0; rr < 4; ++rr) {
+        int day = lg * 4 + rr;
+        if (day < Dn) {
+            float inv = 1.f / den[rr];
+            #pragma unroll
+            for (int nt = 0; nt < 4; ++nt)
+                news[((size_t)s * Dn + day) * Hn + nt * 16 + lr] = accv[nt][rr] * inv;
+        }
+    }
+}
+
+__global__ __launch_bounds__(64, 1) void day_finish(
+    const float* __restrict__ news,
+    const float* __restrict__ Wih_s, const float* __restrict__ Whh_s,
+    const float* __restrict__ bih_s, const float* __restrict__ bhh_s,
+    const float* __restrict__ Wa_s, const float* __restrict__ va_s,
+    const float* __restrict__ u, const float* __restrict__ bb,
+    const float* __restrict__ Wq, const float* __restrict__ bq,
+    const float* __restrict__ Wk, const float* __restrict__ bk,
+    const float* __restrict__ Wbl, const float* __restrict__ bbl,
+    float* __restrict__ combined, float* __restrict__ qg,
+    float* __restrict__ kg, float* __restrict__ out1)
+{
+    __shared__ __align__(16) unsigned char sm[60928];
+    unsigned char* whh2 = sm;
+    unsigned char* wih2 = sm + 24576;
+    unsigned char* wa2 = sm + 49152;
+    float* newsL = (float*)(sm + 57600);
+    float* hbuf  = (float*)(sm + 60320);
+
+    const int s = blockIdx.x, l = threadIdx.x;
+    float tvv;
+
+    {
+        const float* W2 = Whh_s + (size_t)s * Hn * G3;
+        const float* X2 = Wih_s + (size_t)s * Hn * G3;
+        for (int r = 0; r < 192; ++r) {
+            int e = l + r * 64, i = e / G3, j = e - i * G3;
+            int off = j * 128 + ((2 * i) ^ ((j & 7) << 4));
+            *(unsigned short*)(whh2 + off) = f2bf(W2[e]);
+            *(unsigned short*)(wih2 + off) = f2bf(X2[e]);
+        }
+        const float* A2 = Wa_s + (size_t)s * Hn * Hn;
+        for (int r = 0; r < 64; ++r) {
+            int e = l + r * 64, i = e >> 6, k = e & 63;
+            *(unsigned short*)(wa2 + k * 128 + ((2 * i) ^ ((k & 7) << 4))) = f2bf(A2[e]);
+        }
+        #pragma unroll
+        for (int d = 0; d < Dn; ++d) newsL[d * 68 + l] = news[((size_t)s * Dn + d) * Hn + l];
+        hbuf[l] = 0.f;
+        if (l < 4) hbuf[64 + l] = 0.f;
+    }
+    __builtin_amdgcn_wave_barrier();
+    {
+        const float bi0 = bih_s[(size_t)s * G3 + l];
+        const float bi1 = bih_s[(size_t)s * G3 + 64 + l];
+        const float bi2 = bih_s[(size_t)s * G3 + 128 + l];
+        const float bh0 = bhh_s[(size_t)s * G3 + l];
+        const float bh1 = bhh_s[(size_t)s * G3 + 64 + l];
+        const float bh2 = bhh_s[(size_t)s * G3 + 128 + l];
+        const float vak = va_s[(size_t)s * Hn + l];
+        const int swl = (l & 7) << 4;
+        float h2 = 0.f, m2 = -1e30f, den2 = 0.f, av2 = 0.f;
+        for (int t = 0; t < Dn; ++t) {
+            float gh0 = bh0, gh1 = bh1, gh2 = bh2;
+            float gg0 = bi0, gg1 = bi1, gg2 = bi2;
+            #pragma unroll
+            for (int ic = 0; ic < 8; ++ic) {
+                const int off = (ic * 16) ^ swl;
+                f4_t hA = *(const f4_t*)&hbuf[ic * 8];
+                f4_t hB = *(const f4_t*)&hbuf[ic * 8 + 4];
+                f4_t nA = *(const f4_t*)&newsL[t * 68 + ic * 8];
+                f4_t nB = *(const f4_t*)&newsL[t * 68 + ic * 8 + 4];
+                uint4 w0 = *(const uint4*)(whh2 + l * 128 + off);
+                uint4 w1 = *(const uint4*)(whh2 + (l + 64) * 128 + off);
+                uint4 w2 = *(const uint4*)(whh2 + (l + 128) * 128 + off);
+                uint4 x0 = *(const uint4*)(wih2 + l * 128 + off);
+                uint4 x1 = *(const uint4*)(wih2 + (l + 64) * 128 + off);
+                uint4 x2 = *(const uint4*)(wih2 + (l + 128) * 128 + off);
+                gh0 += dot8(w0, hA, hB); gh1 += dot8(w1, hA, hB); gh2 += dot8(w2, hA, hB);
+                gg0 += dot8(x0, nA, nB); gg1 += dot8(x1, nA, nB); gg2 += dot8(x2, nA, nB);
+            }
+            float r = sigmoidf_(gg0 + gh0);
+            float z = sigmoidf_(gg1 + gh1);
+            float n = tanhf_(gg2 + r * gh2);
+            h2 = (1.f - z) * n + z * h2;
+            __builtin_amdgcn_wave_barrier();
+            hbuf[l] = h2;
+            __builtin_amdgcn_wave_barrier();
+            float sk = 0.f;
+            #pragma unroll
+            for (int ic = 0; ic < 8; ++ic) {
+                const int off = (ic * 16) ^ swl;
+                uint4 wv = *(const uint4*)(wa2 + l * 128 + off);
+                f4_t hA = *(const f4_t*)&hbuf[ic * 8];
+                f4_t hB = *(const f4_t*)&hbuf[ic * 8 + 4];
+                sk += dot8(wv, hA, hB);
+            }
+            float term = tanhf_(sk) * vak;
+            #pragma unroll
+            for (int off = 32; off; off >>= 1) term += __shfl_xor(term, off);
+            float mn = fmaxf(m2, term);
+            float s0 = __expf(m2 - mn);
+            float p = __expf(term - mn);
+            den2 = den2 * s0 + p;
+            av2 = av2 * s0 + p * h2;
+            m2 = mn;
+        }
+        tvv = av2 / den2;
+    }
+    __builtin_amdgcn_wave_barrier();
+
+    float* uL = (float*)sm;
+    float* tvL = (float*)(sm + 16640);
+    float* cl  = (float*)(sm + 16960);
+    tvL[l] = tvv;
+    const float* ub = u + (size_t)s * 4096;
+    #pragma unroll 8
+    for (int i = 0; i < 64; ++i) uL[i * 65 + l] = ub[i * 64 + l];
+    __builtin_amdgcn_wave_barrier();
+    {
+        float a = bb[s * Hn + l];
+        #pragma unroll 8
+        for (int i = 0; i < 64; ++i) a += tvL[i] * uL[l * 65 + i];
+        float c = tanhf_(a);
+        cl[l] = c;
+        combined[s * Hn + l] = c;
+    }
+    __builtin_amdgcn_wave_barrier();
+    {
+        float aq = bq[l], ak = bk[l];
+        for (int i = 0; i < Hn; i++) {
+            float ci = cl[i];
+            aq += ci * Wq[i * Hn + l];
+            ak += ci * Wk[i * Hn + l];
+        }
+        qg[s * Hn + l] = aq; kg[s * Hn + l] = ak;
+        if (l < 2) {
+            float a = bbl[s * 2 + l];
+            for (int i = 0; i < Hn; i++) a += cl[i] * Wbl[(size_t)s * Hn * 2 + i * 2 + l];
+            out1[s * 2 + l] = tanhf_(a);
+        }
     }
 }
 
@@ -693,24 +734,24 @@
     float* ws = (float*)d_ws;
     float* news     = ws;
     float* xprice   = ws + 320000;
-    float* tvec     = ws + 352000;
     float* combined = ws + 384000;
     float* qg       = ws + 416000;
     float* kg       = ws + 448000;
     float* out1     = ws + 480000;
-    float* gi2      = ws + 481000;
-    unsigned short* wt = (unsigned short*)(ws + 481000 + 38400000);
+    float* u        = ws + 481000;
+    float* gi2      = ws + 2529000;
+    unsigned short* wt = (unsigned short*)(ws + 40929000);
     float* dout = (float*)d_out;
 
-    wih_prep<<<Sn * 24, 256, 0, stream>>>(Wih_t, wt);
-    gi_gemm6<<<Sn * 5, 256, 0, stream>>>(text, wt, bih_t, gi2);
+    prep_fused<<<12500, 256, 0, stream>>>(Wih_t, wt,
+                                          price, Wih_p, Whh_p, bih_p, bhh_p, Wa_p, va_p,
+                                          xprice);
+    main_fused<<<4500, 256, 0, stream>>>(text, wt, bih_t, gi2, Wb, xprice, u);
     gru_text_f<<<Sn, 64, 0, stream>>>(gi2, Whh_t, bhh_t, Wa_t, va_t, news);
-    gru_small_f<<<Sn, 64, 0, stream>>>(news,
-                                       Wih_s, Whh_s, bih_s, bhh_s, Wa_s, va_s,
-                                       price, Wih_p, Whh_p, bih_p, bhh_p, Wa_p, va_p,
-                                       tvec, xprice);
-    bilinear4<<<Sn * 4, 256, 0, stream>>>(Wb, bb, xprice, tvec, combined);
-    qk_proj<<<Sn, 64, 0, stream>>>(combined, Wq, bq, Wk, bk, Wbl, bbl, qg, kg, out1);
+    day_finish<<<Sn, 64, 0, stream>>>(news,
+                                      Wih_s, Whh_s, bih_s, bhh_s, Wa_s, va_s,
+                                      u, bb, Wq, bq, Wk, bk, Wbl, bbl,
+                                      combined, qg, kg, out1);
     mhsa<<<Sn, 256, 0, stream>>>(qg, kg, combined, Wf, bf_, out1, dout);
     loss_k<<<1, 512, 0, stream>>>(dout, label);
 }
```

After: 638.2 us. About the same (-1.0%).
